# Performance work log

Measured on AMD Instinct MI355X. Metric: run time of the kernel, lower is better.

Reference implementation:

```python
import jax, jax.numpy as jnp
import numpy as np

BN_EPS = 1e-5


def setup_inputs() -> dict:
    key = jax.random.key(0)
    ks = jax.random.split(key, 6)
    N, C, T, V, S = 64, 64, 300, 25, 3
    x = jax.random.normal(ks[0], (N, C, T, V), dtype=jnp.float32)
    A = jax.random.uniform(ks[1], (S, V, V), dtype=jnp.float32)
    PA1 = jnp.ones((S, V, V), dtype=jnp.float32)
    PA2 = jax.random.normal(ks[2], (S, V, V), dtype=jnp.float32) * 1e-3
    Wc = jax.random.normal(ks[3], (S, C, C), dtype=jnp.float32) * np.sqrt(2.0 / (C * S))
    bc = jnp.zeros((S, C), dtype=jnp.float32)
    gamma = jnp.ones((C,), dtype=jnp.float32)
    beta = jnp.zeros((C,), dtype=jnp.float32)
    rmean = jnp.zeros((C,), dtype=jnp.float32)
    rvar = jnp.ones((C,), dtype=jnp.float32)
    return {"x": x, "A": A, "PA1": PA1, "PA2": PA2, "Wc": Wc, "bc": bc,
            "gamma": gamma, "beta": beta, "rmean": rmean, "rvar": rvar}


def reference(x, A, PA1, PA2, Wc, bc, gamma, beta, rmean, rvar):
    # x: (N, C, T, V); A/PA1/PA2: (S, V, V); Wc: (S, out_c, in_c); bc: (S, out_c)
    Ae = A * PA1 + PA2  # adaptive adjacency, (S, V, V)
    S = Ae.shape[0]
    y = None
    for i in range(S):  # small fixed loop over graph subsets
        # graph aggregation over joints: (N,C,T,V) @ (V,V) -> (N,C,T,V)
        xa = jnp.einsum('nctv,vw->nctw', x, Ae[i])
        # 1x1 conv over channels + bias
        z = jnp.einsum('nctw,oc->notw', xa, Wc[i]) + bc[i][None, :, None, None]
        y = z if y is None else y + z
    # BatchNorm2d (inference form with running stats)
    scale = gamma / jnp.sqrt(rvar + BN_EPS)
    y = y * scale[None, :, None, None] + (beta - rmean * scale)[None, :, None, None]
    # residual: in_channels == out_channels -> down is identity
    y = y + x
    return jax.nn.relu(y)
```

## Files before the change

kernel.cpp:

```cpp
#include <hip/hip_runtime.h>

typedef _Float16 half_t;
typedef __attribute__((ext_vector_type(8))) _Float16 half8;
typedef __attribute__((ext_vector_type(4))) _Float16 half4;
typedef __attribute__((ext_vector_type(4))) float float4_t;

#define BN_EPS 1e-5f

constexpr int Nn = 64, Cc = 64, Tt = 300, Vv = 25, Ss = 3;
constexpr int TB   = 4;
constexpr int TWN  = TB * Vv;
constexpr int NT   = 7;
constexpr int XL_T = 32;
constexpr int XL_C = TB * XL_T + 8;
constexpr int XA_S = 72;
constexpr int XA_R = NT * 16;
constexpr int AE_S = 40;

__global__ __launch_bounds__(256, 4)
void gcn_fused(const float* __restrict__ x,   const float* __restrict__ A,
               const float* __restrict__ PA1, const float* __restrict__ PA2,
               const float* __restrict__ Wc,  const float* __restrict__ bc,
               const float* __restrict__ gamma, const float* __restrict__ beta,
               const float* __restrict__ rmean, const float* __restrict__ rvar,
               float* __restrict__ out)
{
    __shared__ __align__(16) half_t Xl[Cc * XL_C];
    __shared__ __align__(16) half_t xaL[XA_R * XA_S];
    __shared__ float bnsc[Cc], bnsh[Cc];

    half_t* AeU = xaL;

    const int tid  = threadIdx.x;
    const int lane = tid & 63;
    const int wave = tid >> 6;
    const int col  = lane & 15;
    const int quad = lane >> 4;

    const int tb = blockIdx.x;
    const int n  = blockIdx.y;
    const int t0 = tb * TB;

    if (tid < Cc) {
        float sc   = gamma[tid] * rsqrtf(rvar[tid] + BN_EPS);
        float bsum = bc[tid] + bc[Cc + tid] + bc[2 * Cc + tid];
        bnsc[tid] = sc;
        bnsh[tid] = beta[tid] - rmean[tid] * sc + bsum * sc;
    }

    for (int e = tid; e < Ss * 32 * 32; e += 256) {
        int s = e >> 10, r = e & 1023, w = r >> 5, v = r & 31;
        float val = 0.f;
        if (v < Vv && w < Vv) {
            int ai = (s * Vv + v) * Vv + w;
            val = A[ai] * PA1[ai] + PA2[ai];
        }
        AeU[(s * 32 + w) * AE_S + v] = (half_t)val;
    }

    for (int e = tid; e < (XA_R - TWN) * XA_S; e += 256)
        xaL[TWN * XA_S + e] = (half_t)0.f;

    for (int e = tid; e < Cc * TB * 7; e += 256) {
        int c = e / 28, r = e % 28, t = r / 7, v = 25 + r % 7;
        Xl[c * XL_C + t * XL_T + v] = (half_t)0.f;
    }

    half8 wf[Ss][2];
    {
        int o = wave * 16 + col;
        #pragma unroll
        for (int s = 0; s < Ss; ++s)
            #pragma unroll
            for (int ks = 0; ks < 2; ++ks) {
                const float* p = Wc + (s * Cc + o) * Cc + ks * 32 + quad * 8;
                float4_t a = *(const float4_t*)p;
                float4_t b = *(const float4_t*)(p + 4);
                half8 h;
                #pragma unroll
                for (int j = 0; j < 4; ++j) { h[j] = (half_t)a[j]; h[4 + j] = (half_t)b[j]; }
                wf[s][ks] = h;
            }
    }

    {
        const float* xb = x + (size_t)n * Cc * Tt * Vv + t0 * Vv;
        for (int i = tid; i < Cc * (TWN / 4); i += 256) {
            int c = i / 25, k = i - c * 25;
            float4_t f = *(const float4_t*)(xb + c * (Tt * Vv) + k * 4);
            int p = k * 4;
            #pragma unroll
            for (int j = 0; j < 4; ++j) {
                int g = p + j;
                int t = g / 25, v = g - t * 25;
                Xl[c * XL_C + t * XL_T + v] = (half_t)f[j];
            }
        }
    }
    __syncthreads();

    half8 ab[Ss][2];
    #pragma unroll
    for (int s = 0; s < Ss; ++s)
        #pragma unroll
        for (int wt = 0; wt < 2; ++wt)
            ab[s][wt] = *(const half8*)&AeU[(s * 32 + wt * 16 + col) * AE_S + quad * 8];
    __syncthreads();

    const float4_t zero4 = {0.f, 0.f, 0.f, 0.f};
    float4_t yacc[NT];
    #pragma unroll
    for (int i = 0; i < NT; ++i) yacc[i] = zero4;

    const int t = wave;

    #pragma unroll
    for (int s = 0; s < Ss; ++s) {
        #pragma unroll
        for (int ct = 0; ct < 4; ++ct) {
            half8 af = *(const half8*)&Xl[(ct * 16 + col) * XL_C + t * XL_T + quad * 8];
            #pragma unroll
            for (int wt = 0; wt < 2; ++wt) {
                float4_t r = __builtin_amdgcn_mfma_f32_16x16x32_f16(af, ab[s][wt], zero4, 0, 0, 0);
                int w = wt * 16 + col;
                if (w < Vv) {
                    half4 h;
                    #pragma unroll
                    for (int i2 = 0; i2 < 4; ++i2) h[i2] = (half_t)r[i2];
                    *(half4*)&xaL[(t * Vv + w) * XA_S + ct * 16 + quad * 4] = h;
                }
            }
        }
        __syncthreads();

        #pragma unroll
        for (int nt = 0; nt < NT; ++nt) {
            int tw = nt * 16 + col;
            #pragma unroll
            for (int ks = 0; ks < 2; ++ks) {
                half8 bf = *(const half8*)&xaL[tw * XA_S + ks * 32 + quad * 8];
                yacc[nt] = __builtin_amdgcn_mfma_f32_16x16x32_f16(wf[s][ks], bf, yacc[nt], 0, 0, 0);
            }
        }
        if (s != Ss - 1) __syncthreads();
    }

    float* ob = out + (size_t)n * Cc * Tt * Vv + t0 * Vv;
    #pragma unroll
    for (int nt = 0; nt < NT; ++nt) {
        int tw = nt * 16 + col;
        if (tw < TWN) {
            int tt = tw / 25;
            int w  = tw - tt * 25;
            #pragma unroll
            for (int i = 0; i < 4; ++i) {
                int o = wave * 16 + quad * 4 + i;
                float val = yacc[nt][i] * bnsc[o] + bnsh[o];
                val += (float)Xl[o * XL_C + tt * XL_T + w];
                ob[o * Tt * Vv + tw] = fmaxf(val, 0.f);
            }
        }
    }
}

extern "C" void kernel_launch(void* const* d_in, const int* in_sizes, int n_in,
                              void* d_out, int out_size, void* d_ws, size_t ws_size,
                              hipStream_t stream) {
    const float* x     = (const float*)d_in[0];
    const float* A     = (const float*)d_in[1];
    const float* PA1   = (const float*)d_in[2];
    const float* PA2   = (const float*)d_in[3];
    const float* Wc    = (const float*)d_in[4];
    const float* bc    = (const float*)d_in[5];
    const float* gamma = (const float*)d_in[6];
    const float* beta  = (const float*)d_in[7];
    const float* rmean = (const float*)d_in[8];
    const float* rvar  = (const float*)d_in[9];
    float* out = (float*)d_out;

    dim3 grid(Tt / TB, Nn);
    gcn_fused<<<grid, 256, 0, stream>>>(x, A, PA1, PA2, Wc, bc, gamma, beta, rmean, rvar, out);
}
```

Before: 320.1 us.

## Process five time tiles per block with register prefetch of next tile

Each block now loops over five consecutive time tiles instead of one, so the grid shrinks fivefold. The per-block setup is paid once per five tiles: adjacency build, weight fragment loads and BN constants. The next tile's x data is loaded into registers while the current tile's MFMA work runs, overlapping global latency with compute. This adds register pressure (seven float4 prefetch buffers) under the existing launch bounds and reduces the number of blocks available for latency hiding.

After: 364.3 us. 1.14x slower.

```diff
diff --git a/kernel.cpp b/kernel.cpp
--- a/kernel.cpp
+++ b/kernel.cpp
@@ -9,6 +9,7 @@
 
 constexpr int Nn = 64, Cc = 64, Tt = 300, Vv = 25, Ss = 3;
 constexpr int TB   = 4;
+constexpr int TPB  = 5;
 constexpr int TWN  = TB * Vv;
 constexpr int NT   = 7;
 constexpr int XL_T = 32;
@@ -16,6 +17,7 @@
 constexpr int XA_S = 72;
 constexpr int XA_R = NT * 16;
 constexpr int AE_S = 40;
+constexpr int NPF  = 7;
 
 __global__ __launch_bounds__(256, 4)
 void gcn_fused(const float* __restrict__ x,   const float* __restrict__ A,
@@ -37,9 +39,9 @@
     const int col  = lane & 15;
     const int quad = lane >> 4;
 
-    const int tb = blockIdx.x;
-    const int n  = blockIdx.y;
-    const int t0 = tb * TB;
+    const int g = blockIdx.x;
+    const int n = blockIdx.y;
+    const int tbase = g * (TB * TPB);
 
     if (tid < Cc) {
         float sc   = gamma[tid] * rsqrtf(rvar[tid] + BN_EPS);
@@ -83,18 +85,14 @@
             }
     }
 
-    {
-        const float* xb = x + (size_t)n * Cc * Tt * Vv + t0 * Vv;
-        for (int i = tid; i < Cc * (TWN / 4); i += 256) {
-            int c = i / 25, k = i - c * 25;
-            float4_t f = *(const float4_t*)(xb + c * (Tt * Vv) + k * 4);
-            int p = k * 4;
-            #pragma unroll
-            for (int j = 0; j < 4; ++j) {
-                int g = p + j;
-                int t = g / 25, v = g - t * 25;
-                Xl[c * XL_C + t * XL_T + v] = (half_t)f[j];
-            }
+    const float* xb = x + (size_t)n * Cc * Tt * Vv + tbase * Vv;
+    float4_t pf[NPF];
+    #pragma unroll
+    for (int k = 0; k < NPF; ++k) {
+        int i = tid + k * 256;
+        if (i < Cc * (TWN / 4)) {
+            int c = i / 25, kk = i - c * 25;
+            pf[k] = *(const float4_t*)(xb + c * (Tt * Vv) + kk * 4);
         }
     }
     __syncthreads();
@@ -108,58 +106,90 @@
     __syncthreads();
 
     const float4_t zero4 = {0.f, 0.f, 0.f, 0.f};
-    float4_t yacc[NT];
-    #pragma unroll
-    for (int i = 0; i < NT; ++i) yacc[i] = zero4;
-
     const int t = wave;
 
-    #pragma unroll
-    for (int s = 0; s < Ss; ++s) {
-        #pragma unroll
-        for (int ct = 0; ct < 4; ++ct) {
-            half8 af = *(const half8*)&Xl[(ct * 16 + col) * XL_C + t * XL_T + quad * 8];
-            #pragma unroll
-            for (int wt = 0; wt < 2; ++wt) {
-                float4_t r = __builtin_amdgcn_mfma_f32_16x16x32_f16(af, ab[s][wt], zero4, 0, 0, 0);
-                int w = wt * 16 + col;
-                if (w < Vv) {
-                    half4 h;
-                    #pragma unroll
-                    for (int i2 = 0; i2 < 4; ++i2) h[i2] = (half_t)r[i2];
-                    *(half4*)&xaL[(t * Vv + w) * XA_S + ct * 16 + quad * 4] = h;
+    for (int tile = 0; tile < TPB; ++tile) {
+        #pragma unroll
+        for (int k = 0; k < NPF; ++k) {
+            int i = tid + k * 256;
+            if (i < Cc * (TWN / 4)) {
+                int c = i / 25, kk = i - c * 25;
+                int p = kk * 4;
+                #pragma unroll
+                for (int j = 0; j < 4; ++j) {
+                    int gg = p + j;
+                    int tt = gg / 25, v = gg - tt * 25;
+                    Xl[c * XL_C + tt * XL_T + v] = (half_t)pf[k][j];
                 }
             }
         }
         __syncthreads();
 
+        if (tile + 1 < TPB) {
+            const float* xn = xb + (tile + 1) * TWN;
+            #pragma unroll
+            for (int k = 0; k < NPF; ++k) {
+                int i = tid + k * 256;
+                if (i < Cc * (TWN / 4)) {
+                    int c = i / 25, kk = i - c * 25;
+                    pf[k] = *(const float4_t*)(xn + c * (Tt * Vv) + kk * 4);
+                }
+            }
+        }
+
+        float4_t yacc[NT];
+        #pragma unroll
+        for (int i = 0; i < NT; ++i) yacc[i] = zero4;
+
+        #pragma unroll
+        for (int s = 0; s < Ss; ++s) {
+            #pragma unroll
+            for (int ct = 0; ct < 4; ++ct) {
+                half8 af = *(const half8*)&Xl[(ct * 16 + col) * XL_C + t * XL_T + quad * 8];
+                #pragma unroll
+                for (int wt = 0; wt < 2; ++wt) {
+                    float4_t r = __builtin_amdgcn_mfma_f32_16x16x32_f16(af, ab[s][wt], zero4, 0, 0, 0);
+                    int w = wt * 16 + col;
+                    if (w < Vv) {
+                        half4 h;
+                        #pragma unroll
+                        for (int i2 = 0; i2 < 4; ++i2) h[i2] = (half_t)r[i2];
+                        *(half4*)&xaL[(t * Vv + w) * XA_S + ct * 16 + quad * 4] = h;
+                    }
+                }
+            }
+            __syncthreads();
+
+            #pragma unroll
+            for (int nt = 0; nt < NT; ++nt) {
+                int tw = nt * 16 + col;
+                #pragma unroll
+                for (int ks = 0; ks < 2; ++ks) {
+                    half8 bf = *(const half8*)&xaL[tw * XA_S + ks * 32 + quad * 8];
+                    yacc[nt] = __builtin_amdgcn_mfma_f32_16x16x32_f16(wf[s][ks], bf, yacc[nt], 0, 0, 0);
+                }
+            }
+            if (s != Ss - 1) __syncthreads();
+        }
+
+        float* ob = out + (size_t)n * Cc * Tt * Vv + (tbase + tile * TB) * Vv;
         #pragma unroll
         for (int nt = 0; nt < NT; ++nt) {
             int tw = nt * 16 + col;
-            #pragma unroll
-            for (int ks = 0; ks < 2; ++ks) {
-                half8 bf = *(const half8*)&xaL[tw * XA_S + ks * 32 + quad * 8];
-                yacc[nt] = __builtin_amdgcn_mfma_f32_16x16x32_f16(wf[s][ks], bf, yacc[nt], 0, 0, 0);
-            }
-        }
-        if (s != Ss - 1) __syncthreads();
-    }
-
-    float* ob = out + (size_t)n * Cc * Tt * Vv + t0 * Vv;
-    #pragma unroll
-    for (int nt = 0; nt < NT; ++nt) {
-        int tw = nt * 16 + col;
-        if (tw < TWN) {
-            int tt = tw / 25;
-            int w  = tw - tt * 25;
-            #pragma unroll
-            for (int i = 0; i < 4; ++i) {
-                int o = wave * 16 + quad * 4 + i;
-                float val = yacc[nt][i] * bnsc[o] + bnsh[o];
-                val += (float)Xl[o * XL_C + tt * XL_T + w];
-                ob[o * Tt * Vv + tw] = fmaxf(val, 0.f);
-            }
-        }
+            if (tw < TWN) {
+                int tt = tw / 25;
+                int w  = tw - tt * 25;
+                #pragma unroll
+                for (int i = 0; i < 4; ++i) {
+                    int o = wave * 16 + quad * 4 + i;
+                    float val = yacc[nt][i] * bnsc[o] + bnsh[o];
+                    val += (float)Xl[o * XL_C + tt * XL_T + w];
+                    ob[o * Tt * Vv + tw] = fmaxf(val, 0.f);
+                }
+            }
+        }
+
+        if (tile + 1 < TPB) __syncthreads();
     }
 }
 
@@ -178,6 +208,6 @@
     const float* rvar  = (const float*)d_in[9];
     float* out = (float*)d_out;
 
-    dim3 grid(Tt / TB, Nn);
+    dim3 grid(Tt / (TB * TPB), Nn);
     gcn_fused<<<grid, 256, 0, stream>>>(x, A, PA1, PA2, Wc, bc, gamma, beta, rmean, rvar, out);
 }
```
